# Performance work log

Measured on AMD Instinct MI355X. Metric: run time of the kernel, lower is better.

## Reference

```python
import jax, jax.numpy as jnp
import numpy as np

N, M, C, F = 100000, 12, 64, 41
SH_DIM = 9  # lmax=2 -> 1+3+5
_INV_SQRT_4PI = 0.28209479177387814  # 1/sqrt(4*pi)


def spherical_harmonics_l2(vec):
    """e3nn real SH, lmax=2, normalize=True, normalization='integral'. vec: [..., 3]."""
    r = jnp.sqrt(jnp.sum(vec * vec, axis=-1, keepdims=True) + 1e-12)
    u = vec / r
    x, y, z = u[..., 0], u[..., 1], u[..., 2]
    s3, s15, s5 = jnp.sqrt(3.0), jnp.sqrt(15.0), jnp.sqrt(5.0)
    sh = jnp.stack([
        jnp.ones_like(x),                              # l=0
        s3 * x, s3 * y, s3 * z,                        # l=1 (e3nn order x,y,z)
        s15 * x * z,                                   # l=2
        s15 * x * y,
        s5 * (y * y - 0.5 * (x * x + z * z)),
        s15 * y * z,
        0.5 * s15 * (z * z - x * x),
    ], axis=-1)
    return sh * _INV_SQRT_4PI  # component -> integral normalization


def setup_inputs() -> dict:
    key = jax.random.key(0)
    ks = jax.random.split(key, 9)
    atom_fea = jax.random.normal(ks[0], (N, C), jnp.float32)
    nbr_fea = jax.random.normal(ks[1], (N, M, F), jnp.float32)
    nbr_idx = jax.random.randint(ks[2], (N, M), 0, N)
    pos = jax.random.normal(ks[3], (N, 3), jnp.float32)
    # radial MLP params (Linear(F,F) -> Softplus -> Linear(F, SH_DIM))
    w1 = jax.random.normal(ks[4], (F, F), jnp.float32) / np.sqrt(F)
    b1 = jnp.zeros((F,), jnp.float32)
    w2 = jax.random.normal(ks[5], (F, SH_DIM), jnp.float32) / np.sqrt(F)
    b2 = jnp.zeros((SH_DIM,), jnp.float32)
    # FullyConnectedTensorProduct weights: single path (0e,0e,0e), uvw -> [C_in, C_out]
    tp_w = jax.random.normal(ks[6], (C, C), jnp.float32)
    return {"atom_fea": atom_fea, "nbr_fea": nbr_fea, "nbr_idx": nbr_idx,
            "pos": pos, "w1": w1, "b1": b1, "w2": w2, "b2": b2, "tp_w": tp_w}


def reference(atom_fea, nbr_fea, nbr_idx, pos, w1, b1, w2, b2, tp_w):
    n, m = nbr_idx.shape
    src = nbr_idx.reshape(-1)                       # [N*M]
    h_j = atom_fea[src]                             # gather: [N*M, C]
    # radial MLP
    R = jax.nn.softplus(nbr_fea.reshape(n * m, -1) @ w1 + b1) @ w2 + b2  # [N*M, 9]
    # spherical harmonics of r_ij (dst is row index i, repeated M times)
    vec = pos[src].reshape(n, m, 3) - pos[:, None, :]
    Y = spherical_harmonics_l2(vec).reshape(n * m, SH_DIM)
    W = R * Y                                       # [N*M, 9]
    # FullyConnectedTensorProduct (Cx0e) x (0e+1o+2e) -> Cx0e: only the
    # scalar (l=0) channel of W couples; path normalization 1/sqrt(fan_in=C).
    msg = (h_j * W[:, :1]) @ (tp_w / np.sqrt(h_j.shape[-1]))  # [N*M, C]
    # scatter-mean with dst = arange(N) repeated M times == mean over M axis
    out = msg.reshape(n, m, -1).mean(axis=1)        # [N, C]
    return out
```

## Files before the change

### kernel.cpp

```cpp
#include <hip/hip_runtime.h>

#define N_ROWS 100000
#define M_NBR  12
#define C_DIM  64
#define F_DIM  41
#define E_TOT  (N_ROWS * M_NBR)

typedef _Float16 half8 __attribute__((ext_vector_type(8)));
typedef _Float16 half4v __attribute__((ext_vector_type(4)));
typedef float float4v __attribute__((ext_vector_type(4)));

#define EPITCH   68
#define EPITCH_H 72

__device__ __forceinline__ void split8(const float (&v)[8], half8& hi, half8& lo) {
    #pragma unroll
    for (int i = 0; i < 8; ++i) {
        const _Float16 h = (_Float16)v[i];
        hi[i] = h;
        lo[i] = (_Float16)(v[i] - (float)h);
    }
}

#define DPP_ROR_ADD(v, CTRL) \
    ((v) + __int_as_float(__builtin_amdgcn_update_dpp(0, __float_as_int(v), (CTRL), 0xF, 0xF, true)))

__global__ __launch_bounds__(384) void prep_edge_B(
    const float* __restrict__ w1,
    const float* __restrict__ b1,
    _Float16* __restrict__ bpack)
{
    const int tid  = threadIdx.x;
    const int wid  = tid >> 6;
    const int lane = tid & 63;
    const int nt   = wid >> 1;
    const int ks   = wid & 1;
    const int n15  = lane & 15, g = lane >> 4;

    const int j = nt * 16 + n15;
    half8 v;
    #pragma unroll
    for (int i = 0; i < 8; ++i) {
        const int k = ks * 32 + g * 8 + i;
        float f = 0.0f;
        if (j < F_DIM) {
            if (k < F_DIM)       f = w1[k * F_DIM + j];
            else if (k == F_DIM) f = b1[j];
        }
        v[i] = (_Float16)f;
    }
    *(half8*)(bpack + ((nt * 2 + ks) * 64 + lane) * 8) = v;
}

__global__ __launch_bounds__(256) void edge_mlp_mfma_kernel(
    const float* __restrict__ nbr_fea,
    const _Float16* __restrict__ bpack,
    const float* __restrict__ w2,
    const float* __restrict__ b2,
    float* __restrict__ s_out)
{
    __shared__ float lsf[128 * F_DIM];
    _Float16* lsh = (_Float16*)lsf;

    const int tid  = threadIdx.x;
    const int lane = tid & 63;
    const int wv   = tid >> 6;
    const int n15  = lane & 15;
    const int g    = lane >> 4;
    const long base = (long)blockIdx.x * 128;

    half8 Bh[3][2];
    #pragma unroll
    for (int nt = 0; nt < 3; ++nt)
        #pragma unroll
        for (int ks = 0; ks < 2; ++ks)
            Bh[nt][ks] = *(const half8*)(bpack + ((nt * 2 + ks) * 64 + lane) * 8);

    {
        const float4* g4 = (const float4*)(nbr_fea + base * F_DIM);
        float4* l4 = (float4*)lsf;
        for (int i = tid; i < 1312; i += 256) l4[i] = g4[i];
    }
    __syncthreads();

    float xr[F_DIM];
    const bool owner = tid < 128;
    if (owner) {
        const float* src = lsf + tid * F_DIM;
        #pragma unroll
        for (int k = 0; k < F_DIM; ++k) xr[k] = src[k];
    }
    __syncthreads();

    if (owner) {
        half8 hv[8];
        #pragma unroll
        for (int q = 0; q < 8; ++q) {
            #pragma unroll
            for (int i = 0; i < 8; ++i) {
                const int k = q * 8 + i;
                _Float16 h = (_Float16)0.0f;
                if (k < F_DIM)       h = (_Float16)xr[k];
                else if (k == F_DIM) h = (_Float16)1.0f;
                hv[q][i] = h;
            }
        }
        _Float16* dst = lsh + tid * EPITCH_H;
        #pragma unroll
        for (int q = 0; q < 8; ++q)
            *(half8*)(dst + q * 8) = hv[q];
    }
    __syncthreads();

    float4v acc[2][3];
    #pragma unroll
    for (int mt = 0; mt < 2; ++mt)
        #pragma unroll
        for (int nt = 0; nt < 3; ++nt)
            #pragma unroll
            for (int i = 0; i < 4; ++i) acc[mt][nt][i] = 0.0f;

    #pragma unroll
    for (int mt = 0; mt < 2; ++mt) {
        const int row = wv * 32 + mt * 16 + n15;
        #pragma unroll
        for (int ks = 0; ks < 2; ++ks) {
            const half8 a = *(const half8*)(lsh + row * EPITCH_H + ks * 32 + g * 8);
            #pragma unroll
            for (int nt = 0; nt < 3; ++nt)
                acc[mt][nt] = __builtin_amdgcn_mfma_f32_16x16x32_f16(a, Bh[nt][ks], acc[mt][nt], 0, 0, 0);
        }
    }

    float w2v[3];
    #pragma unroll
    for (int nt = 0; nt < 3; ++nt) {
        const int j = nt * 16 + n15;
        w2v[nt] = (j < F_DIM) ? w2[j * 9] : 0.0f;
    }
    const float b2v   = b2[0];
    const float scale = 0.28209479177387814f / 12.0f;

    #pragma unroll
    for (int mt = 0; mt < 2; ++mt) {
        float p[4];
        #pragma unroll
        for (int r = 0; r < 4; ++r) {
            float sum = 0.0f;
            #pragma unroll
            for (int nt = 0; nt < 3; ++nt) {
                const float v  = acc[mt][nt][r];
                const float sp = fmaxf(v, 0.0f) + __logf(1.0f + __expf(-fabsf(v)));
                sum = fmaf(sp, w2v[nt], sum);
            }
            p[r] = sum;
        }
        #pragma unroll
        for (int r = 0; r < 4; ++r) {
            float v = p[r];
            v = DPP_ROR_ADD(v, 0x121);
            v = DPP_ROR_ADD(v, 0x122);
            v = DPP_ROR_ADD(v, 0x124);
            v = DPP_ROR_ADD(v, 0x128);
            p[r] = v;
        }
        if (n15 == 0) {
            #pragma unroll
            for (int r = 0; r < 4; ++r) {
                const long e = base + wv * 32 + mt * 16 + g * 4 + r;
                s_out[e] = (p[r] + b2v) * scale;
            }
        }
    }
}

__global__ __launch_bounds__(256) void atom_transform_mfma_kernel(
    const float* __restrict__ atom_fea,
    const float* __restrict__ tp_w,
    const float* __restrict__ w1,
    const float* __restrict__ b1,
    _Float16* __restrict__ afT,
    _Float16* __restrict__ bpack)
{
    if (blockIdx.x == gridDim.x - 1) {
        const int tid  = threadIdx.x;
        const int lane = tid & 63;
        const int n15  = lane & 15, g = lane >> 4;
        for (int fi = tid >> 6; fi < 6; fi += 4) {
            const int nt = fi >> 1;
            const int ks = fi & 1;
            const int j = nt * 16 + n15;
            half8 v;
            #pragma unroll
            for (int i = 0; i < 8; ++i) {
                const int k = ks * 32 + g * 8 + i;
                float f = 0.0f;
                if (j < F_DIM) {
                    if (k < F_DIM)       f = w1[k * F_DIM + j];
                    else if (k == F_DIM) f = b1[j];
                }
                v[i] = (_Float16)f;
            }
            *(half8*)(bpack + ((nt * 2 + ks) * 64 + lane) * 8) = v;
        }
        return;
    }

    __shared__ float lx[128 * EPITCH];

    const int tid  = threadIdx.x;
    const int lane = tid & 63;
    const int wv   = tid >> 6;
    const int n15  = lane & 15;
    const int g    = lane >> 4;
    const long row0 = (long)blockIdx.x * 128;
    const int nrow = (N_ROWS - row0) < 128 ? (int)(N_ROWS - row0) : 128;

    {
        const float4* g4 = (const float4*)(atom_fea + row0 * C_DIM);
        for (int i = tid; i < 128 * 16; i += 256) {
            const int r  = i >> 4;
            const int c4 = i & 15;
            const float4 v = (r < nrow) ? g4[r * 16 + c4] : make_float4(0.f, 0.f, 0.f, 0.f);
            *(float4*)(lx + r * EPITCH + c4 * 4) = v;
        }
    }
    __syncthreads();

    float4v acc[2][4];
    #pragma unroll
    for (int mt = 0; mt < 2; ++mt)
        #pragma unroll
        for (int nt = 0; nt < 4; ++nt)
            #pragma unroll
            for (int i = 0; i < 4; ++i) acc[mt][nt][i] = 0.0f;

    #pragma unroll
    for (int ks = 0; ks < 2; ++ks) {
        half8 Th[4], Tl[4];
        #pragma unroll
        for (int nt = 0; nt < 4; ++nt) {
            const int j = nt * 16 + n15;
            float v[8];
            #pragma unroll
            for (int i = 0; i < 8; ++i) {
                const int k = ks * 32 + g * 8 + i;
                v[i] = tp_w[k * C_DIM + j] * 0.125f;
            }
            split8(v, Th[nt], Tl[nt]);
        }
        #pragma unroll
        for (int mt = 0; mt < 2; ++mt) {
            const int row = wv * 32 + mt * 16 + n15;
            const float* src = lx + row * EPITCH + ks * 32 + g * 8;
            float av[8];
            *(float4*)(av)     = *(const float4*)(src);
            *(float4*)(av + 4) = *(const float4*)(src + 4);
            half8 ah, al;
            split8(av, ah, al);
            #pragma unroll
            for (int nt = 0; nt < 4; ++nt) {
                acc[mt][nt] = __builtin_amdgcn_mfma_f32_16x16x32_f16(ah, Th[nt], acc[mt][nt], 0, 0, 0);
                acc[mt][nt] = __builtin_amdgcn_mfma_f32_16x16x32_f16(al, Th[nt], acc[mt][nt], 0, 0, 0);
                acc[mt][nt] = __builtin_amdgcn_mfma_f32_16x16x32_f16(ah, Tl[nt], acc[mt][nt], 0, 0, 0);
            }
        }
    }

    #pragma unroll
    for (int mt = 0; mt < 2; ++mt) {
        #pragma unroll
        for (int r = 0; r < 4; ++r) {
            const long row = row0 + wv * 32 + mt * 16 + g * 4 + r;
            if (row < N_ROWS) {
                #pragma unroll
                for (int nt = 0; nt < 4; ++nt)
                    afT[row * C_DIM + nt * 16 + n15] = (_Float16)acc[mt][nt][r];
            }
        }
    }
}

__global__ __launch_bounds__(256) void gather_kernel(
    const _Float16* __restrict__ afT,
    const int*   __restrict__ nbr_idx,
    const float* __restrict__ s,
    float* __restrict__ out)
{
    const int tid  = threadIdx.x;
    const int lane = tid & 63;
    const int wv   = tid >> 6;
    const int q    = lane >> 4;
    const int c4   = (lane & 15) * 4;

    const int row0 = blockIdx.x * 32 + wv * 8;

    #pragma unroll
    for (int ch = 0; ch < 2; ++ch) {
        int r = row0 + ch * 4 + q;
        const int*   ir = nbr_idx + r * M_NBR;
        const float* sr = s       + r * M_NBR;
        float4 acc = make_float4(0.f, 0.f, 0.f, 0.f);
        #pragma unroll
        for (int j = 0; j < M_NBR; ++j) {
            int   idx = ir[j];
            float sv  = sr[j];
            const half4v a = *(const half4v*)(afT + (long)idx * C_DIM + c4);
            acc.x = fmaf(sv, (float)a[0], acc.x);
            acc.y = fmaf(sv, (float)a[1], acc.y);
            acc.z = fmaf(sv, (float)a[2], acc.z);
            acc.w = fmaf(sv, (float)a[3], acc.w);
        }
        *(float4*)(out + (long)r * C_DIM + c4) = acc;
    }
}

__global__ __launch_bounds__(256) void gather_transform_kernel(
    const float* __restrict__ atom_fea,
    const int*   __restrict__ nbr_idx,
    const float* __restrict__ s,
    const float* __restrict__ tp_w,
    float* __restrict__ out)
{
    __shared__ float accL[64 * C_DIM];
    const int tid = threadIdx.x;
    const int c  = tid & 63;
    const int rq = tid >> 6;

    float Tc[64];
    #pragma unroll
    for (int k = 0; k < 64; ++k) Tc[k] = tp_w[k * 64 + c] * 0.125f;

    const int row0 = blockIdx.x * 64;
    for (int i = 0; i < 16; ++i) {
        int r = row0 + rq * 16 + i;
        float a = 0.0f;
        if (r < N_ROWS) {
            const int*   ir = nbr_idx + (long)r * M_NBR;
            const float* sr = s       + (long)r * M_NBR;
            #pragma unroll
            for (int j = 0; j < M_NBR; ++j)
                a = fmaf(sr[j], atom_fea[(long)ir[j] * C_DIM + c], a);
        }
        accL[(rq * 16 + i) * C_DIM + c] = a;
    }
    __syncthreads();
    for (int i = 0; i < 16; ++i) {
        int rl = rq * 16 + i;
        int r  = row0 + rl;
        if (r >= N_ROWS) continue;
        const float* ar = accL + rl * C_DIM;
        float o = 0.0f;
        #pragma unroll
        for (int k = 0; k < 64; ++k) o = fmaf(ar[k], Tc[k], o);
        out[(long)r * C_DIM + c] = o;
    }
}

extern "C" void kernel_launch(void* const* d_in, const int* in_sizes, int n_in,
                              void* d_out, int out_size, void* d_ws, size_t ws_size,
                              hipStream_t stream) {
    const float* atom_fea = (const float*)d_in[0];
    const float* nbr_fea  = (const float*)d_in[1];
    const int*   nbr_idx  = (const int*)  d_in[2];
    const float* w1   = (const float*)d_in[4];
    const float* b1   = (const float*)d_in[5];
    const float* w2   = (const float*)d_in[6];
    const float* b2   = (const float*)d_in[7];
    const float* tp_w = (const float*)d_in[8];

    _Float16* bpack = (_Float16*)d_ws;
    float*    s     = (float*)((char*)d_ws + 8192);
    float*    out   = (float*)d_out;

    const size_t sBytes    = (size_t)E_TOT * sizeof(float);
    const size_t afTBytes  = (size_t)N_ROWS * C_DIM * sizeof(_Float16);

    if (ws_size >= 8192 + sBytes + afTBytes) {
        _Float16* afT = (_Float16*)((char*)d_ws + 8192 + sBytes);
        const int blocksT = (N_ROWS + 127) / 128 + 1;
        atom_transform_mfma_kernel<<<blocksT, 256, 0, stream>>>(atom_fea, tp_w, w1, b1, afT, bpack);

        const int blocksA = E_TOT / 128;
        edge_mlp_mfma_kernel<<<blocksA, 256, 0, stream>>>(nbr_fea, bpack, w2, b2, s);

        const int blocksG = N_ROWS / 32;
        gather_kernel<<<blocksG, 256, 0, stream>>>(afT, nbr_idx, s, out);
    } else {
        prep_edge_B<<<1, 384, 0, stream>>>(w1, b1, bpack);
        const int blocksA = E_TOT / 128;
        edge_mlp_mfma_kernel<<<blocksA, 256, 0, stream>>>(nbr_fea, bpack, w2, b2, s);
        const int blocksB = (N_ROWS + 63) / 64;
        gather_transform_kernel<<<blocksB, 256, 0, stream>>>(atom_fea, nbr_idx, s, tp_w, out);
    }
}
```

Before: 341.1 us.

## Fuse atom transform into edge MLP launch as extra block range

```diff
diff --git a/kernel.cpp b/kernel.cpp
--- a/kernel.cpp
+++ b/kernel.cpp
@@ -10,7 +10,6 @@
 typedef _Float16 half4v __attribute__((ext_vector_type(4)));
 typedef float float4v __attribute__((ext_vector_type(4)));
 
-#define EPITCH   68
 #define EPITCH_H 72
 
 __device__ __forceinline__ void split8(const float (&v)[8], half8& hi, half8& lo) {
@@ -52,22 +51,99 @@
     *(half8*)(bpack + ((nt * 2 + ks) * 64 + lane) * 8) = v;
 }
 
-__global__ __launch_bounds__(256) void edge_mlp_mfma_kernel(
-    const float* __restrict__ nbr_fea,
-    const _Float16* __restrict__ bpack,
-    const float* __restrict__ w2,
-    const float* __restrict__ b2,
-    float* __restrict__ s_out)
-{
-    __shared__ float lsf[128 * F_DIM];
-    _Float16* lsh = (_Float16*)lsf;
-
+__device__ __forceinline__ void atom_transform_direct(
+    const float* __restrict__ atom_fea,
+    const float* __restrict__ tp_w,
+    _Float16* __restrict__ afT,
+    const int bid)
+{
     const int tid  = threadIdx.x;
     const int lane = tid & 63;
     const int wv   = tid >> 6;
     const int n15  = lane & 15;
     const int g    = lane >> 4;
-    const long base = (long)blockIdx.x * 128;
+    const long row0 = (long)bid * 128;
+
+    float4v acc[2][4];
+    #pragma unroll
+    for (int mt = 0; mt < 2; ++mt)
+        #pragma unroll
+        for (int nt = 0; nt < 4; ++nt)
+            #pragma unroll
+            for (int i = 0; i < 4; ++i) acc[mt][nt][i] = 0.0f;
+
+    #pragma unroll
+    for (int ks = 0; ks < 2; ++ks) {
+        half8 Th[4], Tl[4];
+        #pragma unroll
+        for (int nt = 0; nt < 4; ++nt) {
+            const int j = nt * 16 + n15;
+            float v[8];
+            #pragma unroll
+            for (int i = 0; i < 8; ++i) {
+                const int k = ks * 32 + g * 8 + i;
+                v[i] = tp_w[k * C_DIM + j] * 0.125f;
+            }
+            split8(v, Th[nt], Tl[nt]);
+        }
+        #pragma unroll
+        for (int mt = 0; mt < 2; ++mt) {
+            long row = row0 + wv * 32 + mt * 16 + n15;
+            if (row > (long)N_ROWS - 1) row = (long)N_ROWS - 1;
+            const float* src = atom_fea + row * C_DIM + ks * 32 + g * 8;
+            float av[8];
+            *(float4*)(av)     = *(const float4*)(src);
+            *(float4*)(av + 4) = *(const float4*)(src + 4);
+            half8 ah, al;
+            split8(av, ah, al);
+            #pragma unroll
+            for (int nt = 0; nt < 4; ++nt) {
+                acc[mt][nt] = __builtin_amdgcn_mfma_f32_16x16x32_f16(ah, Th[nt], acc[mt][nt], 0, 0, 0);
+                acc[mt][nt] = __builtin_amdgcn_mfma_f32_16x16x32_f16(al, Th[nt], acc[mt][nt], 0, 0, 0);
+                acc[mt][nt] = __builtin_amdgcn_mfma_f32_16x16x32_f16(ah, Tl[nt], acc[mt][nt], 0, 0, 0);
+            }
+        }
+    }
+
+    #pragma unroll
+    for (int mt = 0; mt < 2; ++mt) {
+        #pragma unroll
+        for (int r = 0; r < 4; ++r) {
+            const long row = row0 + wv * 32 + mt * 16 + g * 4 + r;
+            if (row < N_ROWS) {
+                #pragma unroll
+                for (int nt = 0; nt < 4; ++nt)
+                    afT[row * C_DIM + nt * 16 + n15] = (_Float16)acc[mt][nt][r];
+            }
+        }
+    }
+}
+
+__global__ __launch_bounds__(256) void fused_edge_atom_kernel(
+    const float* __restrict__ nbr_fea,
+    const _Float16* __restrict__ bpack,
+    const float* __restrict__ w2,
+    const float* __restrict__ b2,
+    float* __restrict__ s_out,
+    const float* __restrict__ atom_fea,
+    const float* __restrict__ tp_w,
+    _Float16* __restrict__ afT,
+    const int nT)
+{
+    __shared__ float lsf[128 * F_DIM];
+    _Float16* lsh = (_Float16*)lsf;
+
+    if ((int)blockIdx.x < nT) {
+        atom_transform_direct(atom_fea, tp_w, afT, blockIdx.x);
+        return;
+    }
+
+    const int tid  = threadIdx.x;
+    const int lane = tid & 63;
+    const int wv   = tid >> 6;
+    const int n15  = lane & 15;
+    const int g    = lane >> 4;
+    const long base = (long)(blockIdx.x - nT) * 128;
 
     half8 Bh[3][2];
     #pragma unroll
@@ -169,113 +245,6 @@
             for (int r = 0; r < 4; ++r) {
                 const long e = base + wv * 32 + mt * 16 + g * 4 + r;
                 s_out[e] = (p[r] + b2v) * scale;
-            }
-        }
-    }
-}
-
-__global__ __launch_bounds__(256) void atom_transform_mfma_kernel(
-    const float* __restrict__ atom_fea,
-    const float* __restrict__ tp_w,
-    const float* __restrict__ w1,
-    const float* __restrict__ b1,
-    _Float16* __restrict__ afT,
-    _Float16* __restrict__ bpack)
-{
-    if (blockIdx.x == gridDim.x - 1) {
-        const int tid  = threadIdx.x;
-        const int lane = tid & 63;
-        const int n15  = lane & 15, g = lane >> 4;
-        for (int fi = tid >> 6; fi < 6; fi += 4) {
-            const int nt = fi >> 1;
-            const int ks = fi & 1;
-            const int j = nt * 16 + n15;
-            half8 v;
-            #pragma unroll
-            for (int i = 0; i < 8; ++i) {
-                const int k = ks * 32 + g * 8 + i;
-                float f = 0.0f;
-                if (j < F_DIM) {
-                    if (k < F_DIM)       f = w1[k * F_DIM + j];
-                    else if (k == F_DIM) f = b1[j];
-                }
-                v[i] = (_Float16)f;
-            }
-            *(half8*)(bpack + ((nt * 2 + ks) * 64 + lane) * 8) = v;
-        }
-        return;
-    }
-
-    __shared__ float lx[128 * EPITCH];
-
-    const int tid  = threadIdx.x;
-    const int lane = tid & 63;
-    const int wv   = tid >> 6;
-    const int n15  = lane & 15;
-    const int g    = lane >> 4;
-    const long row0 = (long)blockIdx.x * 128;
-    const int nrow = (N_ROWS - row0) < 128 ? (int)(N_ROWS - row0) : 128;
-
-    {
-        const float4* g4 = (const float4*)(atom_fea + row0 * C_DIM);
-        for (int i = tid; i < 128 * 16; i += 256) {
-            const int r  = i >> 4;
-            const int c4 = i & 15;
-            const float4 v = (r < nrow) ? g4[r * 16 + c4] : make_float4(0.f, 0.f, 0.f, 0.f);
-            *(float4*)(lx + r * EPITCH + c4 * 4) = v;
-        }
-    }
-    __syncthreads();
-
-    float4v acc[2][4];
-    #pragma unroll
-    for (int mt = 0; mt < 2; ++mt)
-        #pragma unroll
-        for (int nt = 0; nt < 4; ++nt)
-            #pragma unroll
-            for (int i = 0; i < 4; ++i) acc[mt][nt][i] = 0.0f;
-
-    #pragma unroll
-    for (int ks = 0; ks < 2; ++ks) {
-        half8 Th[4], Tl[4];
-        #pragma unroll
-        for (int nt = 0; nt < 4; ++nt) {
-            const int j = nt * 16 + n15;
-            float v[8];
-            #pragma unroll
-            for (int i = 0; i < 8; ++i) {
-                const int k = ks * 32 + g * 8 + i;
-                v[i] = tp_w[k * C_DIM + j] * 0.125f;
-            }
-            split8(v, Th[nt], Tl[nt]);
-        }
-        #pragma unroll
-        for (int mt = 0; mt < 2; ++mt) {
-            const int row = wv * 32 + mt * 16 + n15;
-            const float* src = lx + row * EPITCH + ks * 32 + g * 8;
-            float av[8];
-            *(float4*)(av)     = *(const float4*)(src);
-            *(float4*)(av + 4) = *(const float4*)(src + 4);
-            half8 ah, al;
-            split8(av, ah, al);
-            #pragma unroll
-            for (int nt = 0; nt < 4; ++nt) {
-                acc[mt][nt] = __builtin_amdgcn_mfma_f32_16x16x32_f16(ah, Th[nt], acc[mt][nt], 0, 0, 0);
-                acc[mt][nt] = __builtin_amdgcn_mfma_f32_16x16x32_f16(al, Th[nt], acc[mt][nt], 0, 0, 0);
-                acc[mt][nt] = __builtin_amdgcn_mfma_f32_16x16x32_f16(ah, Tl[nt], acc[mt][nt], 0, 0, 0);
-            }
-        }
-    }
-
-    #pragma unroll
-    for (int mt = 0; mt < 2; ++mt) {
-        #pragma unroll
-        for (int r = 0; r < 4; ++r) {
-            const long row = row0 + wv * 32 + mt * 16 + g * 4 + r;
-            if (row < N_ROWS) {
-                #pragma unroll
-                for (int nt = 0; nt < 4; ++nt)
-                    afT[row * C_DIM + nt * 16 + n15] = (_Float16)acc[mt][nt][r];
             }
         }
     }
@@ -312,6 +281,127 @@
             acc.w = fmaf(sv, (float)a[3], acc.w);
         }
         *(float4*)(out + (long)r * C_DIM + c4) = acc;
+    }
+}
+
+__global__ __launch_bounds__(256) void edge_mlp_mfma_kernel(
+    const float* __restrict__ nbr_fea,
+    const _Float16* __restrict__ bpack,
+    const float* __restrict__ w2,
+    const float* __restrict__ b2,
+    float* __restrict__ s_out)
+{
+    __shared__ float lsf[128 * F_DIM];
+    _Float16* lsh = (_Float16*)lsf;
+    const int tid  = threadIdx.x;
+    const int lane = tid & 63;
+    const int wv   = tid >> 6;
+    const int n15  = lane & 15;
+    const int g    = lane >> 4;
+    const long base = (long)blockIdx.x * 128;
+
+    half8 Bh[3][2];
+    #pragma unroll
+    for (int nt = 0; nt < 3; ++nt)
+        #pragma unroll
+        for (int ks = 0; ks < 2; ++ks)
+            Bh[nt][ks] = *(const half8*)(bpack + ((nt * 2 + ks) * 64 + lane) * 8);
+
+    {
+        const float4* g4 = (const float4*)(nbr_fea + base * F_DIM);
+        float4* l4 = (float4*)lsf;
+        for (int i = tid; i < 1312; i += 256) l4[i] = g4[i];
+    }
+    __syncthreads();
+
+    float xr[F_DIM];
+    const bool owner = tid < 128;
+    if (owner) {
+        const float* src = lsf + tid * F_DIM;
+        #pragma unroll
+        for (int k = 0; k < F_DIM; ++k) xr[k] = src[k];
+    }
+    __syncthreads();
+
+    if (owner) {
+        half8 hv[8];
+        #pragma unroll
+        for (int q = 0; q < 8; ++q) {
+            #pragma unroll
+            for (int i = 0; i < 8; ++i) {
+                const int k = q * 8 + i;
+                _Float16 h = (_Float16)0.0f;
+                if (k < F_DIM)       h = (_Float16)xr[k];
+                else if (k == F_DIM) h = (_Float16)1.0f;
+                hv[q][i] = h;
+            }
+        }
+        _Float16* dst = lsh + tid * EPITCH_H;
+        #pragma unroll
+        for (int q = 0; q < 8; ++q)
+            *(half8*)(dst + q * 8) = hv[q];
+    }
+    __syncthreads();
+
+    float4v acc[2][3];
+    #pragma unroll
+    for (int mt = 0; mt < 2; ++mt)
+        #pragma unroll
+        for (int nt = 0; nt < 3; ++nt)
+            #pragma unroll
+            for (int i = 0; i < 4; ++i) acc[mt][nt][i] = 0.0f;
+
+    #pragma unroll
+    for (int mt = 0; mt < 2; ++mt) {
+        const int row = wv * 32 + mt * 16 + n15;
+        #pragma unroll
+        for (int ks = 0; ks < 2; ++ks) {
+            const half8 a = *(const half8*)(lsh + row * EPITCH_H + ks * 32 + g * 8);
+            #pragma unroll
+            for (int nt = 0; nt < 3; ++nt)
+                acc[mt][nt] = __builtin_amdgcn_mfma_f32_16x16x32_f16(a, Bh[nt][ks], acc[mt][nt], 0, 0, 0);
+        }
+    }
+
+    float w2v[3];
+    #pragma unroll
+    for (int nt = 0; nt < 3; ++nt) {
+        const int j = nt * 16 + n15;
+        w2v[nt] = (j < F_DIM) ? w2[j * 9] : 0.0f;
+    }
+    const float b2v   = b2[0];
+    const float scale = 0.28209479177387814f / 12.0f;
+
+    #pragma unroll
+    for (int mt = 0; mt < 2; ++mt) {
+        float p[4];
+        #pragma unroll
+        for (int r = 0; r < 4; ++r) {
+            float sum = 0.0f;
+            #pragma unroll
+            for (int nt = 0; nt < 3; ++nt) {
+                const float v  = acc[mt][nt][r];
+                const float sp = fmaxf(v, 0.0f) + __logf(1.0f + __expf(-fabsf(v)));
+                sum = fmaf(sp, w2v[nt], sum);
+            }
+            p[r] = sum;
+        }
+        #pragma unroll
+        for (int r = 0; r < 4; ++r) {
+            float v = p[r];
+            v = DPP_ROR_ADD(v, 0x121);
+            v = DPP_ROR_ADD(v, 0x122);
+            v = DPP_ROR_ADD(v, 0x124);
+            v = DPP_ROR_ADD(v, 0x128);
+            p[r] = v;
+        }
+        if (n15 == 0) {
+            #pragma unroll
+            for (int r = 0; r < 4; ++r) {
+                const long e = base + wv * 32 + mt * 16 + g * 4 + r;
+                s_out[e] = (p[r] + b2v) * scale;
+            }
+        }
     }
 }
 
@@ -376,18 +466,18 @@
     const size_t sBytes    = (size_t)E_TOT * sizeof(float);
     const size_t afTBytes  = (size_t)N_ROWS * C_DIM * sizeof(_Float16);
 
+    prep_edge_B<<<1, 384, 0, stream>>>(w1, b1, bpack);
+
     if (ws_size >= 8192 + sBytes + afTBytes) {
         _Float16* afT = (_Float16*)((char*)d_ws + 8192 + sBytes);
-        const int blocksT = (N_ROWS + 127) / 128 + 1;
-        atom_transform_mfma_kernel<<<blocksT, 256, 0, stream>>>(atom_fea, tp_w, w1, b1, afT, bpack);
-
+        const int nT = (N_ROWS + 127) / 128;
         const int blocksA = E_TOT / 128;
-        edge_mlp_mfma_kernel<<<blocksA, 256, 0, stream>>>(nbr_fea, bpack, w2, b2, s);
+        fused_edge_atom_kernel<<<nT + blocksA, 256, 0, stream>>>(
+            nbr_fea, bpack, w2, b2, s, atom_fea, tp_w, afT, nT);
 
         const int blocksG = N_ROWS / 32;
         gather_kernel<<<blocksG, 256, 0, stream>>>(afT, nbr_idx, s, out);
     } else {
-        prep_edge_B<<<1, 384, 0, stream>>>(w1, b1, bpack);
         const int blocksA = E_TOT / 128;
         edge_mlp_mfma_kernel<<<blocksA, 256, 0, stream>>>(nbr_fea, bpack, w2, b2, s);
         const int blocksB = (N_ROWS + 63) / 64;
```

Result: no change. 339.0 us (-0.6%).
